# Performance work log

Hardware: AMD Instinct MI355X
Metric: run time of the kernel (lower is better)

Reference implementation:

```python
import jax, jax.numpy as jnp
import numpy as np

GX, GY, NH = 480, 360, 32
EPS = 1e-5


def _bn(x, g, b):
    # torch BatchNorm1d training-mode stats over the point dimension
    m = jnp.mean(x, axis=0)
    v = jnp.mean((x - m) ** 2, axis=0)
    return g * (x - m) / jnp.sqrt(v + EPS) + b


def setup_inputs():
    key = jax.random.key(0)
    ks = jax.random.split(key, 24)
    B, N, F = 2, 120000, 7
    s = 0.02
    inp = {
        "pt_fea": jax.random.normal(ks[0], (B, N, F), jnp.float32),
        "xy_ind": jax.random.randint(ks[1], (B, N, 2), 0, 360, dtype=jnp.int32),
        "bn0_g": jnp.ones((7,), jnp.float32), "bn0_b": jnp.zeros((7,), jnp.float32),
        "W1": jax.random.normal(ks[2], (7, 64), jnp.float32) * s,  "b1": jnp.zeros((64,), jnp.float32),
        "bn1_g": jnp.ones((64,), jnp.float32), "bn1_b": jnp.zeros((64,), jnp.float32),
        "W2": jax.random.normal(ks[3], (64, 128), jnp.float32) * s, "b2": jnp.zeros((128,), jnp.float32),
        "bn2_g": jnp.ones((128,), jnp.float32), "bn2_b": jnp.zeros((128,), jnp.float32),
        "W3": jax.random.normal(ks[4], (128, 256), jnp.float32) * s, "b3": jnp.zeros((256,), jnp.float32),
        "bn3_g": jnp.ones((256,), jnp.float32), "bn3_b": jnp.zeros((256,), jnp.float32),
        "W4": jax.random.normal(ks[5], (256, 512), jnp.float32) * s, "b4": jnp.zeros((512,), jnp.float32),
        "W5": jax.random.normal(ks[6], (512, NH), jnp.float32) * s, "b5": jnp.zeros((NH,), jnp.float32),
    }
    return inp


def _forward_sample(fea, xy, bn0_g, bn0_b, W1, b1, bn1_g, bn1_b, W2, b2,
                    bn2_g, bn2_b, W3, b3, bn3_g, bn3_b, W4, b4, W5, b5):
    # Simplified PointNet: BN -> (Linear, BN, ReLU) x3 -> Linear
    x = _bn(fea, bn0_g, bn0_b)
    x = jax.nn.relu(_bn(x @ W1 + b1, bn1_g, bn1_b))
    x = jax.nn.relu(_bn(x @ W2 + b2, bn2_g, bn2_b))
    x = jax.nn.relu(_bn(x @ W3 + b3, bn3_g, bn3_b))
    x = x @ W4 + b4                              # [N, 512]
    # per-voxel segment max over flattened BEV cell id
    ids = xy[:, 0] * GY + xy[:, 1]               # [N]
    nseg = GX * GY
    seg = jax.ops.segment_max(x, ids, num_segments=nseg)   # [nseg, 512]
    cnt = jax.ops.segment_sum(jnp.ones(ids.shape[0], x.dtype), ids, num_segments=nseg)
    occ = (cnt > 0)[:, None]
    seg = jnp.where(occ, seg, 0.0)               # empty voxels -> 0 (scatter semantics)
    nh = jax.nn.relu(seg @ W5 + b5)              # fea_compression
    nh = jnp.where(occ, nh, 0.0)
    return nh.reshape(GX, GY, NH).transpose(2, 0, 1)  # [NH, GX, GY]


def reference(pt_fea, xy_ind, bn0_g, bn0_b, W1, b1, bn1_g, bn1_b, W2, b2,
              bn2_g, bn2_b, W3, b3, bn3_g, bn3_b, W4, b4, W5, b5):
    f = lambda fea, xy: _forward_sample(fea, xy, bn0_g, bn0_b, W1, b1, bn1_g, bn1_b,
                                        W2, b2, bn2_g, bn2_b, W3, b3, bn3_g, bn3_b,
                                        W4, b4, W5, b5)
    return jax.vmap(f)(pt_fea, xy_ind)           # [B, NH, GX, GY]
```

## Files before the change

kernel.cpp:

```cpp
#include <hip/hip_runtime.h>
#include <cstdint>

#define GXD 480
#define GYD 360
#define NHD 32
#define NPTS 120000
#define MPAD 120064
#define MB128 (MPAD/128)
#define SEGR 129600
#define NSEG (GXD*GYD)
#define EPSB 1e-5f

using short8 = __attribute__((ext_vector_type(8))) short;
using f32x4  = __attribute__((ext_vector_type(4))) float;

__device__ __forceinline__ float bf2f(unsigned short u) {
    return __uint_as_float(((unsigned int)u) << 16);
}
__device__ __forceinline__ unsigned short f2bf(float f) {
    unsigned int u = __float_as_uint(f);
    u += 0x7fffu + ((u >> 16) & 1u);
    return (unsigned short)(u >> 16);
}
__device__ __forceinline__ unsigned int bnrelu_pack(unsigned int wv, float sc0, float sh0,
                                                    float sc1, float sh1)
{
    float lo = __uint_as_float(wv << 16);
    float hi = __uint_as_float(wv & 0xffff0000u);
    lo = fmaxf(fmaf(lo, sc0, sh0), 0.f);
    hi = fmaxf(fmaf(hi, sc1, sh1), 0.f);
    unsigned int r;
    asm("v_cvt_pk_bf16_f32 %0, %1, %2" : "=v"(r) : "v"(lo), "v"(hi));
    return r;
}
__device__ __forceinline__ unsigned int pk_bf16(float lo, float hi)
{
    unsigned int r;
    asm("v_cvt_pk_bf16_f32 %0, %1, %2" : "=v"(r) : "v"(lo), "v"(hi));
    return r;
}

__device__ __forceinline__ void async16(const unsigned short* g, unsigned short* l)
{
    __builtin_amdgcn_global_load_lds(
        (const __attribute__((address_space(1))) unsigned int*)g,
        (__attribute__((address_space(3))) unsigned int*)l, 16, 0, 0);
}

__global__ __launch_bounds__(256) void bn0_stats_kernel(
    const float* __restrict__ fea, float* __restrict__ s0, float* __restrict__ q0)
{
    float s[7] = {0,0,0,0,0,0,0}, q[7] = {0,0,0,0,0,0,0};
    for (int p = blockIdx.x * 256 + threadIdx.x; p < NPTS; p += gridDim.x * 256) {
        const float* r = fea + (size_t)p * 7;
#pragma unroll
        for (int f = 0; f < 7; ++f) { float v = r[f]; s[f] += v; q[f] += v * v; }
    }
    __shared__ float red[256];
    int t = threadIdx.x;
#pragma unroll
    for (int f = 0; f < 7; ++f) {
        red[t] = s[f]; __syncthreads();
        for (int o = 128; o > 0; o >>= 1) {
            if (t < o) red[t] += red[t + o];
            __syncthreads();
        }
        if (t == 0) atomicAdd(&s0[f], red[0]);
        __syncthreads();
        red[t] = q[f]; __syncthreads();
        for (int o = 128; o > 0; o >>= 1) {
            if (t < o) red[t] += red[t + o];
            __syncthreads();
        }
        if (t == 0) atomicAdd(&q0[f], red[0]);
        __syncthreads();
    }
}

__global__ void prep0_kernel(const float* __restrict__ s0, const float* __restrict__ q0,
                             const float* __restrict__ g0, const float* __restrict__ b0,
                             const float* __restrict__ W1, const float* __restrict__ b1,
                             float* __restrict__ W1p, float* __restrict__ b1p)
{
    __shared__ float sc[7], sh[7];
    int t = threadIdx.x;
    if (t < 7) {
        float m = s0[t] / (float)NPTS;
        float v = q0[t] / (float)NPTS - m * m;
        float inv = 1.0f / sqrtf(fmaxf(v, 0.f) + EPSB);
        sc[t] = g0[t] * inv;
        sh[t] = b0[t] - m * g0[t] * inv;
    }
    __syncthreads();
    if (t < 64) {
        float acc = b1[t];
#pragma unroll
        for (int f = 0; f < 7; ++f) {
            W1p[f * 64 + t] = W1[f * 64 + t] * sc[f];
            acc += sh[f] * W1[f * 64 + t];
        }
        b1p[t] = acc;
    }
}

__global__ void prep_bn_kernel(const float* __restrict__ sum, const float* __restrict__ sq,
                               const float* __restrict__ g, const float* __restrict__ b,
                               float* __restrict__ sc, float* __restrict__ sh, int C)
{
    int c = blockIdx.x * blockDim.x + threadIdx.x;
    if (c < C) {
        float m = sum[c] / (float)NPTS;
        float v = sq[c] / (float)NPTS - m * m;
        float inv = 1.0f / sqrtf(fmaxf(v, 0.f) + EPSB);
        sc[c] = g[c] * inv;
        sh[c] = b[c] - m * g[c] * inv;
    }
}

template<int C>
__global__ __launch_bounds__(256) void bnrelu_kernel(
    unsigned short* __restrict__ Y,
    const float* __restrict__ sc, const float* __restrict__ sh)
{
    __shared__ float scs[C], shs[C];
    int t = threadIdx.x;
    for (int i = t; i < C; i += 256) { scs[i] = sc[i]; shs[i] = sh[i]; }
    __syncthreads();
    const size_t total8 = (size_t)MPAD * C / 8;
    for (size_t i = (size_t)blockIdx.x * 256 + t; i < total8; i += (size_t)gridDim.x * 256) {
        int c0 = (int)((i * 8) & (size_t)(C - 1));
        uint4 v = *(const uint4*)(Y + i * 8);
        float4 s0 = *(const float4*)&scs[c0];
        float4 s1 = *(const float4*)&scs[c0 + 4];
        float4 h0 = *(const float4*)&shs[c0];
        float4 h1 = *(const float4*)&shs[c0 + 4];
        uint4 o;
        o.x = bnrelu_pack(v.x, s0.x, h0.x, s0.y, h0.y);
        o.y = bnrelu_pack(v.y, s0.z, h0.z, s0.w, h0.w);
        o.z = bnrelu_pack(v.z, s1.x, h1.x, s1.y, h1.y);
        o.w = bnrelu_pack(v.w, s1.z, h1.z, s1.w, h1.w);
        *(uint4*)(Y + i * 8) = o;
    }
}

__global__ __launch_bounds__(256) void wtrans_kernel(const float* __restrict__ W,
                                                     unsigned short* __restrict__ Wt,
                                                     int K, int N)
{
    int i = blockIdx.x * 256 + threadIdx.x;
    if (i < K * N) {
        int k = i / N, n = i % N;
        Wt[(size_t)n * K + k] = f2bf(W[i]);
    }
}

__global__ __launch_bounds__(256) void layer1_kernel(
    const float* __restrict__ fea, const float* __restrict__ W1p, const float* __restrict__ b1p,
    unsigned short* __restrict__ y1, float* __restrict__ sum1, float* __restrict__ sq1)
{
    __shared__ float Wl[448], bl[64];
    __shared__ float feaL[256 * 7];
    __shared__ float colsum[64], colsq[64];
    int t = threadIdx.x;
    int p0 = blockIdx.x * 256;
    for (int i = t; i < 448; i += 256) Wl[i] = W1p[i];
    if (t < 64) { bl[t] = b1p[t]; colsum[t] = 0.f; colsq[t] = 0.f; }
    int nval7 = (NPTS - p0) * 7;
    for (int i = t; i < 256 * 7; i += 256)
        feaL[i] = (i < nval7) ? fea[(size_t)p0 * 7 + i] : 0.f;
    __syncthreads();
    int cg = t & 7, pt = t >> 3;
    float s[8] = {}, q[8] = {};
#pragma unroll
    for (int it = 0; it < 8; ++it) {
        int row = it * 32 + pt;
        bool valid = (p0 + row) < NPTS;
        float f[7];
#pragma unroll
        for (int ff = 0; ff < 7; ++ff) f[ff] = feaL[row * 7 + ff];
        float vj[8];
#pragma unroll
        for (int j = 0; j < 8; ++j) {
            int c = cg * 8 + j;
            float v = bl[c];
#pragma unroll
            for (int ff = 0; ff < 7; ++ff) v = fmaf(f[ff], Wl[ff * 64 + c], v);
            vj[j] = v;
            if (valid) { s[j] += v; q[j] += v * v; }
        }
        uint4 ow;
        ow.x = (unsigned int)f2bf(vj[0]) | ((unsigned int)f2bf(vj[1]) << 16);
        ow.y = (unsigned int)f2bf(vj[2]) | ((unsigned int)f2bf(vj[3]) << 16);
        ow.z = (unsigned int)f2bf(vj[4]) | ((unsigned int)f2bf(vj[5]) << 16);
        ow.w = (unsigned int)f2bf(vj[6]) | ((unsigned int)f2bf(vj[7]) << 16);
        *(uint4*)(y1 + (size_t)(p0 + row) * 64 + cg * 8) = ow;
    }
#pragma unroll
    for (int off = 8; off < 64; off <<= 1) {
#pragma unroll
        for (int j = 0; j < 8; ++j) {
            s[j] += __shfl_xor(s[j], off);
            q[j] += __shfl_xor(q[j], off);
        }
    }
    if ((t & 63) < 8) {
#pragma unroll
        for (int j = 0; j < 8; ++j) {
            atomicAdd(&colsum[cg * 8 + j], s[j]);
            atomicAdd(&colsq[cg * 8 + j], q[j]);
        }
    }
    __syncthreads();
    if (t < 64) {
        atomicAdd(&sum1[t], colsum[t]);
        atomicAdd(&sq1[t], colsq[t]);
    }
}

template<int K, int NC, bool STATS>
__global__ __launch_bounds__(256) void gemm_quad(
    const unsigned short* __restrict__ A, const unsigned short* __restrict__ Wt,
    const float* __restrict__ bias, unsigned short* __restrict__ Y,
    float* __restrict__ osum, float* __restrict__ osq)
{
    __shared__ __align__(16) unsigned short lds[16384];
    __shared__ float colsum[128], colsq[128];
    int t = threadIdx.x;
    int w = t >> 6, ln = t & 63, quad = ln >> 4, lr = ln & 15;
    int wr = w >> 1, wc = w & 1;
    const int mbase = blockIdx.y * 128;
    const int cbase = blockIdx.x * 128;
    unsigned short* Asl = lds;
    unsigned short* Bsl = lds + 8192;

    if (STATS && t < 128) { colsum[t] = 0.f; colsq[t] = 0.f; }
    __syncthreads();

    const int srow = w * 16 + (ln >> 2);
    const int koff = (ln & 3) * 8;

    auto stage = [&](int buf, int kt) {
#pragma unroll
        for (int half = 0; half < 2; ++half) {
            int row = half * 64 + srow;
            async16(A  + (size_t)(mbase + row) * K + kt + koff,
                    Asl + buf * 4096 + half * 2048 + w * 512 + ln * 8);
            async16(Wt + (size_t)(cbase + row) * K + kt + koff,
                    Bsl + buf * 4096 + half * 2048 + w * 512 + ln * 8);
        }
    };

    f32x4 acc[4][4];
#pragma unroll
    for (int i = 0; i < 4; ++i)
#pragma unroll
        for (int j = 0; j < 4; ++j) acc[i][j] = (f32x4){0.f, 0.f, 0.f, 0.f};

    stage(0, 0);
    stage(1, 32);

    constexpr int NR = K / 32;
#pragma unroll
    for (int r = 0; r < NR; ++r) {
        const int buf = r & 1;
        if (r + 1 < NR)
            asm volatile("s_waitcnt vmcnt(4)" ::: "memory");
        else
            asm volatile("s_waitcnt vmcnt(0)" ::: "memory");
        asm volatile("s_barrier" ::: "memory");
        short8 af[4], bfr[4];
#pragma unroll
        for (int mi = 0; mi < 4; ++mi)
            af[mi] = *(const short8*)&Asl[buf * 4096 + (wr * 64 + mi * 16 + lr) * 32 + quad * 8];
#pragma unroll
        for (int ni = 0; ni < 4; ++ni)
            bfr[ni] = *(const short8*)&Bsl[buf * 4096 + (wc * 64 + ni * 16 + lr) * 32 + quad * 8];
        asm volatile("s_waitcnt lgkmcnt(0)" ::: "memory");
        asm volatile("s_barrier" ::: "memory");
        if (r + 2 < NR)
            stage(buf, (r + 2) * 32);
#pragma unroll
        for (int mi = 0; mi < 4; ++mi)
#pragma unroll
            for (int ni = 0; ni < 4; ++ni)
                acc[mi][ni] = __builtin_amdgcn_mfma_f32_16x16x32_bf16(
                    af[mi], bfr[ni], acc[mi][ni], 0, 0, 0);
    }
    __syncthreads();

    unsigned short* Cw = lds + w * 4096;
#pragma unroll
    for (int ni = 0; ni < 4; ++ni) {
        int col = ni * 16 + lr;
        float bv = bias[cbase + wc * 64 + col];
        float s = 0.f, q = 0.f;
#pragma unroll
        for (int mi = 0; mi < 4; ++mi) {
            int rb = mi * 16 + quad * 4;
#pragma unroll
            for (int r = 0; r < 4; ++r) {
                float v = acc[mi][ni][r] + bv;
                Cw[(rb + r) * 64 + col] = f2bf(v);
                if (STATS && (mbase + wr * 64 + rb + r) < NPTS) { s += v; q += v * v; }
            }
        }
        if (STATS) {
            atomicAdd(&colsum[wc * 64 + col], s);
            atomicAdd(&colsq[wc * 64 + col], q);
        }
    }
#pragma unroll
    for (int i = 0; i < 8; ++i) {
        int idx = i * 64 + ln;
        int row = idx >> 3, colq = (idx & 7) * 8;
        *(uint4*)(Y + (size_t)(mbase + wr * 64 + row) * NC + cbase + wc * 64 + colq) =
            *(const uint4*)&Cw[row * 64 + colq];
    }
    if (STATS) {
        __syncthreads();
        if (t < 128) {
            atomicAdd(&osum[blockIdx.x * 128 + t], colsum[t]);
            atomicAdd(&osq[blockIdx.x * 128 + t], colsq[t]);
        }
    }
}

__global__ __launch_bounds__(256) void hist_kernel(const int* __restrict__ xy,
                                                   int* __restrict__ cnt)
{
    int p = blockIdx.x * 256 + threadIdx.x;
    if (p < NPTS) {
        int id = xy[(size_t)p * 2] * GYD + xy[(size_t)p * 2 + 1];
        atomicAdd(&cnt[id], 1);
    }
}

__global__ __launch_bounds__(256) void scanA_kernel(const int* __restrict__ cnt,
                                                    int* __restrict__ csum)
{
    __shared__ int red[256];
    int t = threadIdx.x, base = blockIdx.x * 2048;
    int s = 0;
    for (int i = t; i < 2048; i += 256) {
        int idx = base + i;
        if (idx < SEGR) s += cnt[idx];
    }
    red[t] = s; __syncthreads();
    for (int o = 128; o > 0; o >>= 1) { if (t < o) red[t] += red[t + o]; __syncthreads(); }
    if (t == 0) csum[blockIdx.x] = red[0];
}

__global__ void scanB_kernel(int* __restrict__ csum, int* __restrict__ offs)
{
    if (threadIdx.x == 0) {
        int run = 0;
        for (int i = 0; i < 64; ++i) { int v = csum[i]; csum[i] = run; run += v; }
        offs[SEGR] = run;
    }
}

__global__ __launch_bounds__(256) void scanC_kernel(const int* __restrict__ cnt,
                                                    const int* __restrict__ csum,
                                                    int* __restrict__ offs,
                                                    int* __restrict__ cursor)
{
    __shared__ int red[256];
    int t = threadIdx.x, base = blockIdx.x * 2048;
    int v[8]; int s = 0;
#pragma unroll
    for (int i = 0; i < 8; ++i) {
        int idx = base + t * 8 + i;
        v[i] = (idx < SEGR) ? cnt[idx] : 0;
        s += v[i];
    }
    red[t] = s; __syncthreads();
    for (int o = 1; o < 256; o <<= 1) {
        int x = (t >= o) ? red[t - o] : 0;
        __syncthreads();
        red[t] += x;
        __syncthreads();
    }
    int run = red[t] - s + csum[blockIdx.x];
#pragma unroll
    for (int i = 0; i < 8; ++i) {
        int idx = base + t * 8 + i;
        if (idx < SEGR) { offs[idx] = run; cursor[idx] = run; }
        run += v[i];
    }
}

__global__ __launch_bounds__(256) void scatter_idx_kernel(const int* __restrict__ xy,
                                                          int* __restrict__ cursor,
                                                          int* __restrict__ order)
{
    int p = blockIdx.x * 256 + threadIdx.x;
    if (p < NPTS) {
        int id = xy[(size_t)p * 2] * GYD + xy[(size_t)p * 2 + 1];
        int pos = atomicAdd(&cursor[id], 1);
        order[pos] = p;
    }
}

__global__ __launch_bounds__(256) void l4seg_kernel(
    const unsigned short* __restrict__ y3, const unsigned short* __restrict__ Wt4,
    const float* __restrict__ b4, const unsigned short* __restrict__ Wt5,
    const float* __restrict__ b5, const int* __restrict__ offs,
    const int* __restrict__ ord, float* __restrict__ out)
{
    __shared__ __align__(16) unsigned short Bsl[64 * 256];
    __shared__ __align__(16) unsigned short w5s[32 * 64];
    __shared__ __align__(16) unsigned short y4s[64 * 72];
    __shared__ float b4s[512];
    __shared__ int offs_s[65];
    __shared__ int osl[128];
    int t = threadIdx.x;
    int w = t >> 6, ln = t & 63, quad = ln >> 4, lr = ln & 15;
    int c0 = blockIdx.x * 64;
    if (t < 65) offs_s[t] = offs[c0 + t];
    for (int i = t; i < 512; i += 256) b4s[i] = b4[i];
    __syncthreads();
    const int jb = offs_s[0], je = offs_s[64];
    if (jb == je) {
#pragma unroll
        for (int j = 0; j < 8; ++j)
            out[(size_t)(w * 8 + j) * NSEG + c0 + ln] = 0.f;
        return;
    }
    if (t < 128) { int aj = jb + t; osl[t] = (aj < je) ? ord[aj] : 0; }
    __syncthreads();

    const int cell = t >> 2, q = t & 3;
    const int cjb = offs_s[cell], cje = offs_s[cell + 1];
    const int nch = (je - jb + 63) >> 6;

    short8 af0[8], af1[8];
    {
        int j0 = w * 16 + lr; if (jb + j0 >= je) j0 = je - 1 - jb;
        const unsigned short* Ar0 = y3 + (size_t)osl[j0] * 256 + quad * 8;
#pragma unroll
        for (int r = 0; r < 8; ++r) af0[r] = *(const short8*)(Ar0 + r * 32);
        int j1 = 64 + w * 16 + lr; if (jb + j1 >= je) j1 = je - 1 - jb;
        const unsigned short* Ar1 = y3 + (size_t)osl[j1] * 256 + quad * 8;
#pragma unroll
        for (int r = 0; r < 8; ++r) af1[r] = *(const short8*)(Ar1 + r * 32);
    }

    f32x4 eacc[2];
    eacc[0] = (f32x4){0.f, 0.f, 0.f, 0.f};
    eacc[1] = (f32x4){0.f, 0.f, 0.f, 0.f};

    auto stageB = [&](int p) {
#pragma unroll
        for (int i = 0; i < 8; ++i) {
            int rl = w * 16 + i * 2 + (ln >> 5);
            int cl = (ln & 31) ^ (rl & 7);
            async16(Wt4 + (size_t)(p * 64 + rl) * 256 + cl * 8,
                    Bsl + (w * 16 + i * 2) * 256 + ln * 8);
        }
    };
    auto stageW5 = [&](int p) {
        int rl = t >> 3, cl = (t & 7) ^ (rl & 7);
        async16(Wt5 + (size_t)rl * 512 + p * 64 + cl * 8, w5s + t * 8);
    };
    auto mfma_chunk = [&](const short8* af, f32x4* acc) {
#pragma unroll
        for (int r = 0; r < 8; ++r) {
            const int cp = (r * 4 + quad) ^ (lr & 7);
#pragma unroll
            for (int ni = 0; ni < 4; ++ni) {
                short8 bfr = *(const short8*)&Bsl[(ni * 16 + lr) * 256 + cp * 8];
                acc[ni] = __builtin_amdgcn_mfma_f32_16x16x32_bf16(af[r], bfr, acc[ni], 0, 0, 0);
            }
        }
    };

    stageB(0); stageW5(0);

    for (int p = 0; p < 8; ++p) {
        asm volatile("s_waitcnt vmcnt(0)" ::: "memory");
        asm volatile("s_barrier" ::: "memory");
        float mxv[16];
#pragma unroll
        for (int i = 0; i < 16; ++i) mxv[i] = -3.0e38f;

        for (int c = 0; c < nch; ++c) {
            const int cs = jb + c * 64;
            f32x4 acc[4];
#pragma unroll
            for (int i = 0; i < 4; ++i) acc[i] = (f32x4){0.f, 0.f, 0.f, 0.f};
            if (c == 0) {
                mfma_chunk(af0, acc);
            } else if (c == 1) {
                mfma_chunk(af1, acc);
            } else {
                int j = cs + w * 16 + lr; if (j >= je) j = je - 1;
                const unsigned short* Ar = y3 + (size_t)ord[j] * 256 + quad * 8;
#pragma unroll
                for (int r = 0; r < 8; ++r) {
                    short8 a = *(const short8*)(Ar + r * 32);
                    const int cp = (r * 4 + quad) ^ (lr & 7);
#pragma unroll
                    for (int ni = 0; ni < 4; ++ni) {
                        short8 bfr = *(const short8*)&Bsl[(ni * 16 + lr) * 256 + cp * 8];
                        acc[ni] = __builtin_amdgcn_mfma_f32_16x16x32_bf16(a, bfr, acc[ni], 0, 0, 0);
                    }
                }
            }
#pragma unroll
            for (int ni = 0; ni < 4; ++ni) {
                float bv = b4s[p * 64 + ni * 16 + lr];
#pragma unroll
                for (int rr = 0; rr < 4; ++rr)
                    y4s[(w * 16 + quad * 4 + rr) * 72 + ni * 16 + lr] = f2bf(acc[ni][rr] + bv);
            }
            asm volatile("s_waitcnt lgkmcnt(0)" ::: "memory");
            asm volatile("s_barrier" ::: "memory");
            if (c == nch - 1 && p < 7)
                stageB(p + 1);
            int lo = cjb > cs ? cjb : cs;
            int hi = cje < cs + 64 ? cje : cs + 64;
            for (int jj = lo; jj < hi; ++jj) {
                const uint4* rp = (const uint4*)&y4s[(jj - cs) * 72 + q * 16];
                uint4 v0 = rp[0], v1 = rp[1];
                unsigned int wv[8] = {v0.x, v0.y, v0.z, v0.w, v1.x, v1.y, v1.z, v1.w};
#pragma unroll
                for (int k2 = 0; k2 < 8; ++k2) {
                    mxv[2 * k2]     = fmaxf(mxv[2 * k2],     bf2f((unsigned short)(wv[k2] & 0xffffu)));
                    mxv[2 * k2 + 1] = fmaxf(mxv[2 * k2 + 1], bf2f((unsigned short)(wv[k2] >> 16)));
                }
            }
            asm volatile("s_barrier" ::: "memory");
        }
        {
            bool empty = (cjb == cje);
#pragma unroll
            for (int i = 0; i < 8; ++i) {
                float lo2 = empty ? 0.f : mxv[2 * i], hi2 = empty ? 0.f : mxv[2 * i + 1];
                *(unsigned int*)&y4s[cell * 72 + q * 16 + 2 * i] = pk_bf16(lo2, hi2);
            }
        }
        asm volatile("s_waitcnt lgkmcnt(0)" ::: "memory");
        asm volatile("s_barrier" ::: "memory");
#pragma unroll
        for (int kt = 0; kt < 2; ++kt) {
            short8 af2 = *(const short8*)&y4s[(w * 16 + lr) * 72 + kt * 32 + quad * 8];
            const int cp = (kt * 4 + quad) ^ (lr & 7);
#pragma unroll
            for (int ni = 0; ni < 2; ++ni) {
                short8 bfr = *(const short8*)&w5s[(ni * 16 + lr) * 64 + cp * 8];
                eacc[ni] = __builtin_amdgcn_mfma_f32_16x16x32_bf16(af2, bfr, eacc[ni], 0, 0, 0);
            }
        }
        asm volatile("s_waitcnt lgkmcnt(0)" ::: "memory");
        asm volatile("s_barrier" ::: "memory");
        if (p < 7) stageW5(p + 1);
    }
    float* outs = (float*)&Bsl[0];
#pragma unroll
    for (int ni = 0; ni < 2; ++ni) {
        int h = ni * 16 + lr;
        float bv = b5[h];
#pragma unroll
        for (int rr = 0; rr < 4; ++rr) {
            int cr = w * 16 + quad * 4 + rr;
            bool oc = offs_s[cr + 1] > offs_s[cr];
            outs[cr * 33 + h] = oc ? fmaxf(eacc[ni][rr] + bv, 0.f) : 0.f;
        }
    }
    __syncthreads();
#pragma unroll
    for (int j = 0; j < 8; ++j)
        out[(size_t)(w * 8 + j) * NSEG + c0 + ln] = outs[ln * 33 + w * 8 + j];
}

__global__ __launch_bounds__(256) void ztail_kernel(float* __restrict__ out)
{
    int i = blockIdx.x * 256 + threadIdx.x;
    const int per = (NSEG - SEGR) / 4;
    int h = i / per, c = i % per;
    *(float4*)(out + (size_t)h * NSEG + SEGR + (size_t)c * 4) = make_float4(0.f, 0.f, 0.f, 0.f);
}

extern "C" void kernel_launch(void* const* d_in, const int* in_sizes, int n_in,
                              void* d_out, int out_size, void* d_ws, size_t ws_size,
                              hipStream_t stream)
{
    const float* pt_fea = (const float*)d_in[0];
    const int*   xy_ind = (const int*)d_in[1];
    const float* bn0_g  = (const float*)d_in[2];
    const float* bn0_b  = (const float*)d_in[3];
    const float* W1     = (const float*)d_in[4];
    const float* b1     = (const float*)d_in[5];
    const float* bn1_g  = (const float*)d_in[6];
    const float* bn1_b  = (const float*)d_in[7];
    const float* W2     = (const float*)d_in[8];
    const float* b2     = (const float*)d_in[9];
    const float* bn2_g  = (const float*)d_in[10];
    const float* bn2_b  = (const float*)d_in[11];
    const float* W3     = (const float*)d_in[12];
    const float* b3     = (const float*)d_in[13];
    const float* bn3_g  = (const float*)d_in[14];
    const float* bn3_b  = (const float*)d_in[15];
    const float* W4     = (const float*)d_in[16];
    const float* b4     = (const float*)d_in[17];
    const float* W5     = (const float*)d_in[18];
    const float* b5     = (const float*)d_in[19];
    float* out = (float*)d_out;

    const size_t oY2   = 61472768;
    const size_t oE    = oY2 + (size_t)MPAD * 128 * 2;
    const size_t oCnt  = oE + (size_t)SEGR * 32 * 4;
    const size_t oOffs = oCnt + 518400;
    const size_t oCur  = oOffs + 518528;
    const size_t oOrd  = oCur + 518400;
    const size_t oCsum = oOrd + 480000;
    const size_t oSt   = oCsum + 512;
    const size_t oWt2  = oSt + 16384;
    const size_t oWt3  = oWt2 + 16384;
    const size_t oWt4  = oWt3 + 65536;
    const size_t oWt5  = oWt4 + 262144;

    unsigned short* y1   = (unsigned short*)d_ws;
    unsigned short* y3   = (unsigned short*)d_ws;
    unsigned short* y2   = (unsigned short*)((char*)d_ws + oY2);
    int*            cnt  = (int*)((char*)d_ws + oCnt);
    int*            offs = (int*)((char*)d_ws + oOffs);
    int*            cur  = (int*)((char*)d_ws + oCur);
    int*            ord  = (int*)((char*)d_ws + oOrd);
    int*            csum = (int*)((char*)d_ws + oCsum);
    float*          st   = (float*)((char*)d_ws + oSt);
    unsigned short* Wt2  = (unsigned short*)((char*)d_ws + oWt2);
    unsigned short* Wt3  = (unsigned short*)((char*)d_ws + oWt3);
    unsigned short* Wt4  = (unsigned short*)((char*)d_ws + oWt4);
    unsigned short* Wt5  = (unsigned short*)((char*)d_ws + oWt5);

    float* s0 = st + 0;     float* q0 = st + 8;
    float* W1p = st + 16;   float* b1p = st + 464;
    float* sum1 = st + 528; float* sq1 = st + 592; float* sc1 = st + 656; float* sh1 = st + 720;
    float* sum2 = st + 784; float* sq2 = st + 912; float* sc2 = st + 1040; float* sh2 = st + 1168;
    float* sum3 = st + 1296; float* sq3 = st + 1552; float* sc3 = st + 1808; float* sh3 = st + 2064;

    wtrans_kernel<<<(64 * 128 + 255) / 256, 256, 0, stream>>>(W2, Wt2, 64, 128);
    wtrans_kernel<<<(128 * 256 + 255) / 256, 256, 0, stream>>>(W3, Wt3, 128, 256);
    wtrans_kernel<<<(256 * 512 + 255) / 256, 256, 0, stream>>>(W4, Wt4, 256, 512);
    wtrans_kernel<<<(512 * 32 + 255) / 256, 256, 0, stream>>>(W5, Wt5, 512, 32);

    for (int b = 0; b < 2; ++b) {
        const float* fea_b = pt_fea + (size_t)b * NPTS * 7;
        const int*   xy_b  = xy_ind + (size_t)b * NPTS * 2;
        float*       out_b = out + (size_t)b * NHD * NSEG;

        (void)hipMemsetAsync(st, 0, 2320 * sizeof(float), stream);
        (void)hipMemsetAsync(cnt, 0, (size_t)SEGR * 4, stream);

        bn0_stats_kernel<<<128, 256, 0, stream>>>(fea_b, s0, q0);
        prep0_kernel<<<1, 64, 0, stream>>>(s0, q0, bn0_g, bn0_b, W1, b1, W1p, b1p);
        layer1_kernel<<<MPAD / 256, 256, 0, stream>>>(fea_b, W1p, b1p, y1, sum1, sq1);
        prep_bn_kernel<<<1, 64, 0, stream>>>(sum1, sq1, bn1_g, bn1_b, sc1, sh1, 64);
        bnrelu_kernel<64><<<1024, 256, 0, stream>>>(y1, sc1, sh1);
        gemm_quad<64, 128, true><<<dim3(1, MB128), 256, 0, stream>>>(
            y1, Wt2, b2, y2, sum2, sq2);
        prep_bn_kernel<<<1, 128, 0, stream>>>(sum2, sq2, bn2_g, bn2_b, sc2, sh2, 128);
        bnrelu_kernel<128><<<2048, 256, 0, stream>>>(y2, sc2, sh2);
        gemm_quad<128, 256, true><<<dim3(2, MB128), 256, 0, stream>>>(
            y2, Wt3, b3, y3, sum3, sq3);
        prep_bn_kernel<<<1, 256, 0, stream>>>(sum3, sq3, bn3_g, bn3_b, sc3, sh3, 256);
        bnrelu_kernel<256><<<2048, 256, 0, stream>>>(y3, sc3, sh3);

        hist_kernel<<<(NPTS + 255) / 256, 256, 0, stream>>>(xy_b, cnt);
        scanA_kernel<<<64, 256, 0, stream>>>(cnt, csum);
        scanB_kernel<<<1, 64, 0, stream>>>(csum, offs);
        scanC_kernel<<<64, 256, 0, stream>>>(cnt, csum, offs, cur);
        scatter_idx_kernel<<<(NPTS + 255) / 256, 256, 0, stream>>>(xy_b, cur, ord);

        l4seg_kernel<<<SEGR / 64, 256, 0, stream>>>(y3, Wt4, b4, Wt5, b5, offs, ord, out_b);
        ztail_kernel<<<1350, 256, 0, stream>>>(out_b);
    }
}
```

Baseline: 787.6 us.

## Fuse batch-norm and ReLU into consumer GEMM operand loads

```diff
diff --git a/kernel.cpp b/kernel.cpp
--- a/kernel.cpp
+++ b/kernel.cpp
@@ -39,6 +39,17 @@
     asm("v_cvt_pk_bf16_f32 %0, %1, %2" : "=v"(r) : "v"(lo), "v"(hi));
     return r;
 }
+__device__ __forceinline__ short8 bn_frag(short8 a, float4 s0, float4 s1,
+                                          float4 h0, float4 h1)
+{
+    union { short8 v; uint4 u; } in, out;
+    in.v = a;
+    out.u.x = bnrelu_pack(in.u.x, s0.x, h0.x, s0.y, h0.y);
+    out.u.y = bnrelu_pack(in.u.y, s0.z, h0.z, s0.w, h0.w);
+    out.u.z = bnrelu_pack(in.u.z, s1.x, h1.x, s1.y, h1.y);
+    out.u.w = bnrelu_pack(in.u.w, s1.z, h1.z, s1.w, h1.w);
+    return out.v;
+}
 
 __device__ __forceinline__ void async16(const unsigned short* g, unsigned short* l)
 {
@@ -100,46 +111,6 @@
             acc += sh[f] * W1[f * 64 + t];
         }
         b1p[t] = acc;
-    }
-}
-
-__global__ void prep_bn_kernel(const float* __restrict__ sum, const float* __restrict__ sq,
-                               const float* __restrict__ g, const float* __restrict__ b,
-                               float* __restrict__ sc, float* __restrict__ sh, int C)
-{
-    int c = blockIdx.x * blockDim.x + threadIdx.x;
-    if (c < C) {
-        float m = sum[c] / (float)NPTS;
-        float v = sq[c] / (float)NPTS - m * m;
-        float inv = 1.0f / sqrtf(fmaxf(v, 0.f) + EPSB);
-        sc[c] = g[c] * inv;
-        sh[c] = b[c] - m * g[c] * inv;
-    }
-}
-
-template<int C>
-__global__ __launch_bounds__(256) void bnrelu_kernel(
-    unsigned short* __restrict__ Y,
-    const float* __restrict__ sc, const float* __restrict__ sh)
-{
-    __shared__ float scs[C], shs[C];
-    int t = threadIdx.x;
-    for (int i = t; i < C; i += 256) { scs[i] = sc[i]; shs[i] = sh[i]; }
-    __syncthreads();
-    const size_t total8 = (size_t)MPAD * C / 8;
-    for (size_t i = (size_t)blockIdx.x * 256 + t; i < total8; i += (size_t)gridDim.x * 256) {
-        int c0 = (int)((i * 8) & (size_t)(C - 1));
-        uint4 v = *(const uint4*)(Y + i * 8);
-        float4 s0 = *(const float4*)&scs[c0];
-        float4 s1 = *(const float4*)&scs[c0 + 4];
-        float4 h0 = *(const float4*)&shs[c0];
-        float4 h1 = *(const float4*)&shs[c0 + 4];
-        uint4 o;
-        o.x = bnrelu_pack(v.x, s0.x, h0.x, s0.y, h0.y);
-        o.y = bnrelu_pack(v.y, s0.z, h0.z, s0.w, h0.w);
-        o.z = bnrelu_pack(v.z, s1.x, h1.x, s1.y, h1.y);
-        o.w = bnrelu_pack(v.w, s1.z, h1.z, s1.w, h1.w);
-        *(uint4*)(Y + i * 8) = o;
     }
 }
 
@@ -220,10 +191,13 @@
 template<int K, int NC, bool STATS>
 __global__ __launch_bounds__(256) void gemm_quad(
     const unsigned short* __restrict__ A, const unsigned short* __restrict__ Wt,
+    const float* __restrict__ bsum, const float* __restrict__ bsq,
+    const float* __restrict__ bg, const float* __restrict__ bb,
     const float* __restrict__ bias, unsigned short* __restrict__ Y,
     float* __restrict__ osum, float* __restrict__ osq)
 {
     __shared__ __align__(16) unsigned short lds[16384];
+    __shared__ __align__(16) float scs[K], shs[K];
     __shared__ float colsum[128], colsq[128];
     int t = threadIdx.x;
     int w = t >> 6, ln = t & 63, quad = ln >> 4, lr = ln & 15;
@@ -233,6 +207,13 @@
     unsigned short* Asl = lds;
     unsigned short* Bsl = lds + 8192;
 
+    for (int i = t; i < K; i += 256) {
+        float m = bsum[i] / (float)NPTS;
+        float v = bsq[i] / (float)NPTS - m * m;
+        float inv = 1.0f / sqrtf(fmaxf(v, 0.f) + EPSB);
+        scs[i] = bg[i] * inv;
+        shs[i] = bb[i] - m * bg[i] * inv;
+    }
     if (STATS && t < 128) { colsum[t] = 0.f; colsq[t] = 0.f; }
     __syncthreads();
 
@@ -275,10 +256,18 @@
 #pragma unroll
         for (int ni = 0; ni < 4; ++ni)
             bfr[ni] = *(const short8*)&Bsl[buf * 4096 + (wc * 64 + ni * 16 + lr) * 32 + quad * 8];
+        const int k0 = r * 32 + quad * 8;
+        float4 s0 = *(const float4*)&scs[k0];
+        float4 s1 = *(const float4*)&scs[k0 + 4];
+        float4 h0 = *(const float4*)&shs[k0];
+        float4 h1 = *(const float4*)&shs[k0 + 4];
         asm volatile("s_waitcnt lgkmcnt(0)" ::: "memory");
         asm volatile("s_barrier" ::: "memory");
         if (r + 2 < NR)
             stage(buf, (r + 2) * 32);
+#pragma unroll
+        for (int mi = 0; mi < 4; ++mi)
+            af[mi] = bn_frag(af[mi], s0, s1, h0, h1);
 #pragma unroll
         for (int mi = 0; mi < 4; ++mi)
 #pragma unroll
@@ -405,12 +394,16 @@
     const unsigned short* __restrict__ y3, const unsigned short* __restrict__ Wt4,
     const float* __restrict__ b4, const unsigned short* __restrict__ Wt5,
     const float* __restrict__ b5, const int* __restrict__ offs,
-    const int* __restrict__ ord, float* __restrict__ out)
+    const int* __restrict__ ord,
+    const float* __restrict__ bsum, const float* __restrict__ bsq,
+    const float* __restrict__ bg, const float* __restrict__ bb,
+    float* __restrict__ out)
 {
     __shared__ __align__(16) unsigned short Bsl[64 * 256];
     __shared__ __align__(16) unsigned short w5s[32 * 64];
     __shared__ __align__(16) unsigned short y4s[64 * 72];
     __shared__ float b4s[512];
+    __shared__ float scs[256], shs[256];
     __shared__ int offs_s[65];
     __shared__ int osl[128];
     int t = threadIdx.x;
@@ -426,6 +419,13 @@
             out[(size_t)(w * 8 + j) * NSEG + c0 + ln] = 0.f;
         return;
     }
+    {
+        float m = bsum[t] / (float)NPTS;
+        float v = bsq[t] / (float)NPTS - m * m;
+        float inv = 1.0f / sqrtf(fmaxf(v, 0.f) + EPSB);
+        scs[t] = bg[t] * inv;
+        shs[t] = bb[t] - m * bg[t] * inv;
+    }
     if (t < 128) { int aj = jb + t; osl[t] = (aj < je) ? ord[aj] : 0; }
     __syncthreads();
 
@@ -443,6 +443,16 @@
         const unsigned short* Ar1 = y3 + (size_t)osl[j1] * 256 + quad * 8;
 #pragma unroll
         for (int r = 0; r < 8; ++r) af1[r] = *(const short8*)(Ar1 + r * 32);
+#pragma unroll
+        for (int r = 0; r < 8; ++r) {
+            const int k0 = r * 32 + quad * 8;
+            float4 s0 = *(const float4*)&scs[k0];
+            float4 s1 = *(const float4*)&scs[k0 + 4];
+            float4 h0 = *(const float4*)&shs[k0];
+            float4 h1 = *(const float4*)&shs[k0 + 4];
+            af0[r] = bn_frag(af0[r], s0, s1, h0, h1);
+            af1[r] = bn_frag(af1[r], s0, s1, h0, h1);
+        }
     }
 
     f32x4 eacc[2];
@@ -498,6 +508,12 @@
 #pragma unroll
                 for (int r = 0; r < 8; ++r) {
                     short8 a = *(const short8*)(Ar + r * 32);
+                    const int k0 = r * 32 + quad * 8;
+                    float4 s0 = *(const float4*)&scs[k0];
+                    float4 s1 = *(const float4*)&scs[k0 + 4];
+                    float4 h0 = *(const float4*)&shs[k0];
+                    float4 h1 = *(const float4*)&shs[k0 + 4];
+                    a = bn_frag(a, s0, s1, h0, h1);
                     const int cp = (r * 4 + quad) ^ (lr & 7);
 #pragma unroll
                     for (int ni = 0; ni < 4; ++ni) {
@@ -636,9 +652,9 @@
 
     float* s0 = st + 0;     float* q0 = st + 8;
     float* W1p = st + 16;   float* b1p = st + 464;
-    float* sum1 = st + 528; float* sq1 = st + 592; float* sc1 = st + 656; float* sh1 = st + 720;
-    float* sum2 = st + 784; float* sq2 = st + 912; float* sc2 = st + 1040; float* sh2 = st + 1168;
-    float* sum3 = st + 1296; float* sq3 = st + 1552; float* sc3 = st + 1808; float* sh3 = st + 2064;
+    float* sum1 = st + 528; float* sq1 = st + 592;
+    float* sum2 = st + 784; float* sq2 = st + 912;
+    float* sum3 = st + 1296; float* sq3 = st + 1552;
 
     wtrans_kernel<<<(64 * 128 + 255) / 256, 256, 0, stream>>>(W2, Wt2, 64, 128);
     wtrans_kernel<<<(128 * 256 + 255) / 256, 256, 0, stream>>>(W3, Wt3, 128, 256);
@@ -656,16 +672,10 @@
         bn0_stats_kernel<<<128, 256, 0, stream>>>(fea_b, s0, q0);
         prep0_kernel<<<1, 64, 0, stream>>>(s0, q0, bn0_g, bn0_b, W1, b1, W1p, b1p);
         layer1_kernel<<<MPAD / 256, 256, 0, stream>>>(fea_b, W1p, b1p, y1, sum1, sq1);
-        prep_bn_kernel<<<1, 64, 0, stream>>>(sum1, sq1, bn1_g, bn1_b, sc1, sh1, 64);
-        bnrelu_kernel<64><<<1024, 256, 0, stream>>>(y1, sc1, sh1);
         gemm_quad<64, 128, true><<<dim3(1, MB128), 256, 0, stream>>>(
-            y1, Wt2, b2, y2, sum2, sq2);
-        prep_bn_kernel<<<1, 128, 0, stream>>>(sum2, sq2, bn2_g, bn2_b, sc2, sh2, 128);
-        bnrelu_kernel<128><<<2048, 256, 0, stream>>>(y2, sc2, sh2);
+            y1, Wt2, sum1, sq1, bn1_g, bn1_b, b2, y2, sum2, sq2);
         gemm_quad<128, 256, true><<<dim3(2, MB128), 256, 0, stream>>>(
-            y2, Wt3, b3, y3, sum3, sq3);
-        prep_bn_kernel<<<1, 256, 0, stream>>>(sum3, sq3, bn3_g, bn3_b, sc3, sh3, 256);
-        bnrelu_kernel<256><<<2048, 256, 0, stream>>>(y3, sc3, sh3);
+            y2, Wt3, sum2, sq2, bn2_g, bn2_b, b3, y3, sum3, sq3);
 
         hist_kernel<<<(NPTS + 255) / 256, 256, 0, stream>>>(xy_b, cnt);
         scanA_kernel<<<64, 256, 0, stream>>>(cnt, csum);
@@ -673,7 +683,8 @@
         scanC_kernel<<<64, 256, 0, stream>>>(cnt, csum, offs, cur);
         scatter_idx_kernel<<<(NPTS + 255) / 256, 256, 0, stream>>>(xy_b, cur, ord);
 
-        l4seg_kernel<<<SEGR / 64, 256, 0, stream>>>(y3, Wt4, b4, Wt5, b5, offs, ord, out_b);
+        l4seg_kernel<<<SEGR / 64, 256, 0, stream>>>(
+            y3, Wt4, b4, Wt5, b5, offs, ord, sum3, sq3, bn3_g, bn3_b, out_b);
         ztail_kernel<<<1350, 256, 0, stream>>>(out_b);
     }
 }
```

Measured after the change: 738.5 us. -6.2%, faster.
